# Performance work log

Measured on AMD Instinct MI355X. Metric: run time of the kernel, lower is better.

The kernel has to match this reference:

```python
import jax, jax.numpy as jnp
import numpy as np

BS, CI, NI, CO, NO = 16, 2048, 16, 64, 32
ITERATIONS = 3


def squash(x, axis=2):
    # x * ||x|| / (1 + ||x||^2) along `axis`
    norm = jnp.linalg.norm(x, axis=axis, keepdims=True)
    return x * norm / (1.0 + norm * norm)


def setup_inputs() -> dict:
    key = jax.random.key(0)
    k1, k2 = jax.random.split(key)
    x = jax.random.normal(k1, (BS, CI, NI), dtype=jnp.float32)
    # kaiming-uniform-ish init for weight [ci, ni, co*no]
    bound = float(np.sqrt(6.0 / NI))
    weight = jax.random.uniform(k2, (CI, NI, CO * NO), dtype=jnp.float32,
                                minval=-bound, maxval=bound)
    bias = jnp.full((CO, NO), 0.1, dtype=jnp.float32)
    return {"x": x, "weight": weight, "bias": bias}


def reference(x, weight, bias):
    bs = x.shape[0]
    # votes: (x.unsqueeze(3) * W).sum(2) == einsum over ni -> [bs, ci, co*no]
    votes = jnp.einsum('bci,cik->bck', x, weight).reshape(bs, CI, CO, NO)
    logits = jnp.zeros((bs, CI, CO), dtype=votes.dtype)
    activation = None
    for _ in range(ITERATIONS):
        route = jax.nn.softmax(logits, axis=2)              # [bs, ci, co]
        # s_j = sum_i c_ij * u_hat_{j|i} + bias            # [bs, co, no]
        preactivate = jnp.einsum('bic,bicn->bcn', route, votes) + bias
        activation = squash(preactivate, axis=2)            # [bs, co, no]
        # agreement: sum_n u_hat * v                        # [bs, ci, co]
        distances = jnp.einsum('bicn,bcn->bic', votes, activation)
        logits = logits + distances
    return activation
```

## Files before the change

kernel.cpp:

```cpp
#include <hip/hip_runtime.h>

#define BS 16
#define CI 2048
#define NI 16
#define CO 64
#define NO 32
#define KK 2048
#define NGRP 256

__device__ __forceinline__ void load_lds16(const float* g, float* l) {
    __builtin_amdgcn_global_load_lds(
        (const __attribute__((address_space(1))) void*)g,
        (__attribute__((address_space(3))) void*)l, 16, 0, 0);
}

#define WAITVM12 asm volatile("s_waitcnt vmcnt(12)" ::: "memory")
#define WAITVM4  asm volatile("s_waitcnt vmcnt(4)" ::: "memory")
#define WAITVM0  asm volatile("s_waitcnt vmcnt(0)" ::: "memory")
#define WAITLGKM asm volatile("s_waitcnt lgkmcnt(0)" ::: "memory")
#define BAR __builtin_amdgcn_s_barrier
#define MEMFENCE asm volatile("" ::: "memory")

__device__ __forceinline__ unsigned bf16rne(float f) {
    unsigned u = __float_as_uint(f);
    return (u + 0x7fffu + ((u >> 16) & 1u)) >> 16;
}
__device__ __forceinline__ unsigned pack2(float lo, float hi) {
    return bf16rne(lo) | (bf16rne(hi) << 16);
}

__global__ __launch_bounds__(512, 2) void votes_kernel(
    const float* __restrict__ x,
    const float* __restrict__ w,
    unsigned* __restrict__ votes,
    float* __restrict__ partials)
{
    __shared__ float wbuf[2][4 * KK];
    __shared__ float xb[8][8][NI];

    const int t = threadIdx.x;
    const int phys = blockIdx.x;
    const int xcd = phys & 7;
    const int slot = phys >> 3;
    const int pairid = xcd * 32 + (slot >> 1);
    const int half = slot & 1;
    const int k4 = 4 * t;

    {
        int il = t >> 6, b = (t >> 3) & 7, n0 = (t & 7) * 2;
        int i = pairid + il * NGRP;
        *(float2*)&xb[il][b][n0] =
            *(const float2*)&x[((size_t)(half * 8 + b) * CI + i) * NI + n0];
    }
    __syncthreads();

    float4 acc[8];
#pragma unroll
    for (int b = 0; b < 8; ++b) acc[b] = make_float4(0.f, 0.f, 0.f, 0.f);

    auto issue = [&](int s) {
        int ilp = s >> 2, qp = s & 3;
        const float* gb = w + ((size_t)(pairid + ilp * NGRP) * NI + qp * 4) * KK + k4;
        float* lb = wbuf[s & 1] + k4;
#pragma unroll
        for (int r = 0; r < 4; ++r)
            load_lds16(gb + (size_t)r * KK, lb + r * KK);
    };

    auto computequarter = [&](int il, int q, float4(&dst)[8]) {
#pragma unroll
        for (int rg = 0; rg < 2; ++rg) {
            float4 wA = *(const float4*)&wbuf[q & 1][(2 * rg) * KK + k4];
            float4 wB = *(const float4*)&wbuf[q & 1][(2 * rg + 1) * KK + k4];
#pragma unroll
            for (int b = 0; b < 8; ++b) {
                float2 xv = *(const float2*)&xb[il][b][q * 4 + 2 * rg];
                dst[b].x = fmaf(xv.x, wA.x, dst[b].x);
                dst[b].y = fmaf(xv.x, wA.y, dst[b].y);
                dst[b].z = fmaf(xv.x, wA.z, dst[b].z);
                dst[b].w = fmaf(xv.x, wA.w, dst[b].w);
                dst[b].x = fmaf(xv.y, wB.x, dst[b].x);
                dst[b].y = fmaf(xv.y, wB.y, dst[b].y);
                dst[b].z = fmaf(xv.y, wB.z, dst[b].z);
                dst[b].w = fmaf(xv.y, wB.w, dst[b].w);
            }
        }
    };

    issue(0); issue(1);

#pragma unroll 1
    for (int il = 0; il < 8; ++il) {
        float4 v[8];
#pragma unroll
        for (int b = 0; b < 8; ++b) v[b] = make_float4(0.f, 0.f, 0.f, 0.f);

#pragma unroll
        for (int q = 0; q < 4; ++q) {
            if (q < 2) { if (il > 0) { WAITVM12; } else { WAITVM4; } }
            else if (q == 3) { if (il == 7) { WAITVM0; } else { WAITVM4; } }
            else { WAITVM4; }
            computequarter(il, q, v);
            WAITLGKM;
            if (il < 7 || q < 2) issue(il * 4 + q + 2);
        }

        const size_t vbase = ((size_t)(pairid + il * NGRP) * BS + half * 8) * (KK / 2) + 2 * t;
#pragma unroll
        for (int b = 0; b < 8; ++b) {
            acc[b].x += v[b].x; acc[b].y += v[b].y;
            acc[b].z += v[b].z; acc[b].w += v[b].w;
            uint2 pk;
            pk.x = pack2(v[b].x, v[b].y);
            pk.y = pack2(v[b].z, v[b].w);
            *(uint2*)&votes[vbase + (size_t)b * (KK / 2)] = pk;
        }
        MEMFENCE;
    }

#pragma unroll
    for (int b = 0; b < 8; ++b)
        *(float4*)&partials[((size_t)pairid * BS + half * 8 + b) * KK + k4] = acc[b];
}

#define RILBODY(IL, VC, VN)                                                    \
  {                                                                            \
    const int buf = (IL) & 1;                                                  \
    if ((IL) < 7) {                                                            \
      _Pragma("unroll")                                                        \
      for (int lb = 0; lb < 2; ++lb)                                           \
        VN[lb] = *(const uint4*)&votes[((size_t)(gid + ((IL) + 1) * NGRP) * BS \
                                        + bg0 + lb) * (KK / 2) + 4 * ks];      \
    }                                                                          \
    float dv[2];                                                               \
    _Pragma("unroll")                                                          \
    for (int lb = 0; lb < 2; ++lb) {                                           \
      float4 a0 = *(const float4*)&actb[2 * bh + lb][k8];                      \
      float4 a1 = *(const float4*)&actb[2 * bh + lb][k8 + 4];                  \
      float d = __uint_as_float(VC[lb].x << 16) * a0.x                         \
              + __uint_as_float(VC[lb].x & 0xffff0000u) * a0.y                 \
              + __uint_as_float(VC[lb].y << 16) * a0.z                         \
              + __uint_as_float(VC[lb].y & 0xffff0000u) * a0.w                 \
              + __uint_as_float(VC[lb].z << 16) * a1.x                         \
              + __uint_as_float(VC[lb].z & 0xffff0000u) * a1.y                 \
              + __uint_as_float(VC[lb].w << 16) * a1.z                         \
              + __uint_as_float(VC[lb].w & 0xffff0000u) * a1.w;                \
      d += __shfl_xor(d, 1, 4);                                                \
      d += __shfl_xor(d, 2, 4);                                                \
      dv[lb] = d;                                                              \
    }                                                                          \
    if (j4 == 0) sm[buf][(2 * bh) * 65 + co] = dv[0];                          \
    if (j4 == 1) sm[buf][(2 * bh + 1) * 65 + co] = dv[1];                      \
    WAITLGKM; BAR();                                                           \
    if (t < 256) {                                                             \
      float l0 = sm[buf][(t >> 6) * 65 + (t & 63)];                            \
      if (MODE == 1) lg[(IL)] = l0; else l0 += lg[(IL)];                       \
      float mx = l0;                                                           \
      mx = fmaxf(mx, __shfl_xor(mx, 1, 64));                                   \
      mx = fmaxf(mx, __shfl_xor(mx, 2, 64));                                   \
      mx = fmaxf(mx, __shfl_xor(mx, 4, 64));                                   \
      mx = fmaxf(mx, __shfl_xor(mx, 8, 64));                                   \
      mx = fmaxf(mx, __shfl_xor(mx, 16, 64));                                  \
      mx = fmaxf(mx, __shfl_xor(mx, 32, 64));                                  \
      float e = __expf(l0 - mx);                                               \
      float ssum = e;                                                          \
      ssum += __shfl_xor(ssum, 1, 64);                                         \
      ssum += __shfl_xor(ssum, 2, 64);                                         \
      ssum += __shfl_xor(ssum, 4, 64);                                         \
      ssum += __shfl_xor(ssum, 8, 64);                                         \
      ssum += __shfl_xor(ssum, 16, 64);                                        \
      ssum += __shfl_xor(ssum, 32, 64);                                        \
      sm[buf][(t >> 6) * 65 + (t & 63)] = e / ssum;                            \
      WAITLGKM;                                                                \
    }                                                                          \
    BAR();                                                                     \
    _Pragma("unroll")                                                          \
    for (int lb = 0; lb < 2; ++lb) {                                           \
      float r = sm[buf][(2 * bh + lb) * 65 + co];                              \
      acc[2 * lb + 0].x = fmaf(r, __uint_as_float(VC[lb].x << 16), acc[2 * lb + 0].x); \
      acc[2 * lb + 0].y = fmaf(r, __uint_as_float(VC[lb].x & 0xffff0000u), acc[2 * lb + 0].y); \
      acc[2 * lb + 0].z = fmaf(r, __uint_as_float(VC[lb].y << 16), acc[2 * lb + 0].z); \
      acc[2 * lb + 0].w = fmaf(r, __uint_as_float(VC[lb].y & 0xffff0000u), acc[2 * lb + 0].w); \
      acc[2 * lb + 1].x = fmaf(r, __uint_as_float(VC[lb].z << 16), acc[2 * lb + 1].x); \
      acc[2 * lb + 1].y = fmaf(r, __uint_as_float(VC[lb].z & 0xffff0000u), acc[2 * lb + 1].y); \
      acc[2 * lb + 1].z = fmaf(r, __uint_as_float(VC[lb].w << 16), acc[2 * lb + 1].z); \
      acc[2 * lb + 1].w = fmaf(r, __uint_as_float(VC[lb].w & 0xffff0000u), acc[2 * lb + 1].w); \
    }                                                                          \
  }

template <int MODE>
__global__ __launch_bounds__(512, 2) void route_kernel(
    const unsigned* __restrict__ votes,
    const float* __restrict__ act_in,
    float* __restrict__ logits,
    float* __restrict__ partials)
{
    __shared__ float actb[4][KK];
    __shared__ float sm[2][4 * 65];

    const int t = threadIdx.x;
    const int phys = blockIdx.x;
    const int xcd = phys & 7;
    const int slot = phys >> 3;
    const int gid = xcd * 32 + (slot >> 2);
    const int quarter = slot & 3;

    const int ks = t & 255;
    const int k8 = 8 * ks;
    const int co = ks >> 2;
    const int j4 = ks & 3;
    const int bh = t >> 8;
    const int bg0 = quarter * 4 + 2 * bh;

    {
        int br = t >> 7, e0 = (t & 127) * 16;
#pragma unroll
        for (int r = 0; r < 4; ++r)
            *(float4*)&actb[br][e0 + 4 * r] =
                *(const float4*)&act_in[(size_t)(quarter * 4 + br) * KK + e0 + 4 * r];
    }
    float lg[8];
    if constexpr (MODE == 2) {
        if (t < 256) {
#pragma unroll
            for (int il = 0; il < 8; ++il)
                lg[il] = logits[((size_t)(quarter * 4 + (t >> 6)) * CI + (gid + il * NGRP)) * CO + (t & 63)];
        }
    }
    __syncthreads();

    float4 acc[4];
#pragma unroll
    for (int i = 0; i < 4; ++i) acc[i] = make_float4(0.f, 0.f, 0.f, 0.f);

    uint4 vA[2], vB[2];
#pragma unroll
    for (int lb = 0; lb < 2; ++lb)
        vA[lb] = *(const uint4*)&votes[((size_t)gid * BS + bg0 + lb) * (KK / 2) + 4 * ks];

    RILBODY(0, vA, vB)
    RILBODY(1, vB, vA)
    RILBODY(2, vA, vB)
    RILBODY(3, vB, vA)
    RILBODY(4, vA, vB)
    RILBODY(5, vB, vA)
    RILBODY(6, vA, vB)
    RILBODY(7, vB, vA)

#pragma unroll
    for (int lb = 0; lb < 2; ++lb) {
        float* pp = &partials[((size_t)gid * BS + bg0 + lb) * KK + k8];
        *(float4*)pp = acc[2 * lb];
        *(float4*)(pp + 4) = acc[2 * lb + 1];
    }
    if constexpr (MODE == 1) {
        if (t < 256) {
#pragma unroll
            for (int il = 0; il < 8; ++il)
                logits[((size_t)(quarter * 4 + (t >> 6)) * CI + (gid + il * NGRP)) * CO + (t & 63)] = lg[il];
        }
    }
}

__global__ __launch_bounds__(128) void reduce_squash(
    const float* __restrict__ partials,
    const float* __restrict__ bias,
    float* __restrict__ act_out, float scale)
{
    __shared__ float4 sred[4][32];
    const int t = threadIdx.x;
    const int blk = blockIdx.x;
    const int lane = t & 31;
    const int gp = t >> 5;
    const int o4 = blk * 128 + lane * 4;
    const int b = o4 >> 11;
    const int kk = o4 & (KK - 1);
    const float* p = partials + (size_t)b * KK + kk;
    const size_t stride = (size_t)BS * KK;

    float4 s = make_float4(0.f, 0.f, 0.f, 0.f);
#pragma unroll 4
    for (int g = gp * 64; g < gp * 64 + 64; ++g) {
        float4 v = *(const float4*)(p + (size_t)g * stride);
        s.x += v.x; s.y += v.y; s.z += v.z; s.w += v.w;
    }
    sred[gp][lane] = s;
    __syncthreads();

    if (t < 32) {
        float4 v0 = sred[0][t], v1 = sred[1][t], v2 = sred[2][t], v3 = sred[3][t];
        float4 v;
        v.x = (v0.x + v1.x) + (v2.x + v3.x);
        v.y = (v0.y + v1.y) + (v2.y + v3.y);
        v.z = (v0.z + v1.z) + (v2.z + v3.z);
        v.w = (v0.w + v1.w) + (v2.w + v3.w);
        const int ot = blk * 128 + t * 4;
        float4 bb = *(const float4*)&bias[ot & (KK - 1)];
        v.x = v.x * scale + bb.x;
        v.y = v.y * scale + bb.y;
        v.z = v.z * scale + bb.z;
        v.w = v.w * scale + bb.w;
        float n2 = v.x * v.x + v.y * v.y + v.z * v.z + v.w * v.w;
#pragma unroll
        for (int m = 1; m < 8; m <<= 1) n2 += __shfl_xor(n2, m, 8);
        float norm = sqrtf(n2);
        float sc = norm / (1.f + n2);
        float4 o = make_float4(v.x * sc, v.y * sc, v.z * sc, v.w * sc);
        *(float4*)&act_out[ot] = o;
    }
}

extern "C" void kernel_launch(void* const* d_in, const int* in_sizes, int n_in,
                              void* d_out, int out_size, void* d_ws, size_t ws_size,
                              hipStream_t stream) {
    const float* x = (const float*)d_in[0];
    const float* w = (const float*)d_in[1];
    const float* bias = (const float*)d_in[2];
    float* out = (float*)d_out;

    char* p = (char*)d_ws;
    unsigned* votes = (unsigned*)p; p += (size_t)CI * BS * KK * 2;
    float* partials = (float*)p;    p += (size_t)NGRP * BS * KK * 4;
    float* logits = (float*)p;      p += (size_t)BS * CI * CO * 4;
    float* act1 = (float*)p;        p += (size_t)BS * KK * 4;
    float* act2 = (float*)p;

    votes_kernel<<<2 * NGRP, 512, 0, stream>>>(x, w, votes, partials);
    reduce_squash<<<256, 128, 0, stream>>>(partials, bias, act1, 1.0f / (float)CO);
    route_kernel<1><<<4 * NGRP, 512, 0, stream>>>(votes, act1, logits, partials);
    reduce_squash<<<256, 128, 0, stream>>>(partials, bias, act2, 1.0f);
    route_kernel<2><<<4 * NGRP, 512, 0, stream>>>(votes, act2, logits, partials);
    reduce_squash<<<256, 128, 0, stream>>>(partials, bias, out, 1.0f);
}
```

Before: 192.9 us.

## Drop logits buffer via linearity, split vote sum out, shrink votes LDS staging

Uses the linearity of the routing logits to skip storing and reloading them: the second routing pass recomputes agreement against act1+act2 instead of adding saved logits, which removes a large global write and read. The first-pass sum over inputs moves out of the votes kernel into a separate vote_sum kernel that reads the bf16 votes, so the votes kernel no longer writes partials. The votes kernel also halves its LDS weight staging (two rows per stage instead of four) with adjusted vmcnt waits and asks for higher occupancy in its launch bounds. The trade-off is an extra kernel launch and an extra read pass over votes, and the first iteration's sum is now built from bf16-rounded votes.

```diff
diff --git a/kernel.cpp b/kernel.cpp
--- a/kernel.cpp
+++ b/kernel.cpp
@@ -14,8 +14,8 @@
         (__attribute__((address_space(3))) void*)l, 16, 0, 0);
 }
 
-#define WAITVM12 asm volatile("s_waitcnt vmcnt(12)" ::: "memory")
-#define WAITVM4  asm volatile("s_waitcnt vmcnt(4)" ::: "memory")
+#define WAITVM10 asm volatile("s_waitcnt vmcnt(10)" ::: "memory")
+#define WAITVM2  asm volatile("s_waitcnt vmcnt(2)" ::: "memory")
 #define WAITVM0  asm volatile("s_waitcnt vmcnt(0)" ::: "memory")
 #define WAITLGKM asm volatile("s_waitcnt lgkmcnt(0)" ::: "memory")
 #define BAR __builtin_amdgcn_s_barrier
@@ -28,14 +28,15 @@
 __device__ __forceinline__ unsigned pack2(float lo, float hi) {
     return bf16rne(lo) | (bf16rne(hi) << 16);
 }
-
-__global__ __launch_bounds__(512, 2) void votes_kernel(
+__device__ __forceinline__ float bflo(unsigned u) { return __uint_as_float(u << 16); }
+__device__ __forceinline__ float bfhi(unsigned u) { return __uint_as_float(u & 0xffff0000u); }
+
+__global__ __launch_bounds__(512, 8) void votes_kernel(
     const float* __restrict__ x,
     const float* __restrict__ w,
-    unsigned* __restrict__ votes,
-    float* __restrict__ partials)
+    unsigned* __restrict__ votes)
 {
-    __shared__ float wbuf[2][4 * KK];
+    __shared__ float wbuf[2][2 * KK];
     __shared__ float xb[8][8][NI];
 
     const int t = threadIdx.x;
@@ -54,37 +55,12 @@
     }
     __syncthreads();
 
-    float4 acc[8];
-#pragma unroll
-    for (int b = 0; b < 8; ++b) acc[b] = make_float4(0.f, 0.f, 0.f, 0.f);
-
     auto issue = [&](int s) {
-        int ilp = s >> 2, qp = s & 3;
-        const float* gb = w + ((size_t)(pairid + ilp * NGRP) * NI + qp * 4) * KK + k4;
+        int ilp = s >> 3, qp = s & 7;
+        const float* gb = w + ((size_t)(pairid + ilp * NGRP) * NI + 2 * qp) * KK + k4;
         float* lb = wbuf[s & 1] + k4;
-#pragma unroll
-        for (int r = 0; r < 4; ++r)
-            load_lds16(gb + (size_t)r * KK, lb + r * KK);
-    };
-
-    auto computequarter = [&](int il, int q, float4(&dst)[8]) {
-#pragma unroll
-        for (int rg = 0; rg < 2; ++rg) {
-            float4 wA = *(const float4*)&wbuf[q & 1][(2 * rg) * KK + k4];
-            float4 wB = *(const float4*)&wbuf[q & 1][(2 * rg + 1) * KK + k4];
-#pragma unroll
-            for (int b = 0; b < 8; ++b) {
-                float2 xv = *(const float2*)&xb[il][b][q * 4 + 2 * rg];
-                dst[b].x = fmaf(xv.x, wA.x, dst[b].x);
-                dst[b].y = fmaf(xv.x, wA.y, dst[b].y);
-                dst[b].z = fmaf(xv.x, wA.z, dst[b].z);
-                dst[b].w = fmaf(xv.x, wA.w, dst[b].w);
-                dst[b].x = fmaf(xv.y, wB.x, dst[b].x);
-                dst[b].y = fmaf(xv.y, wB.y, dst[b].y);
-                dst[b].z = fmaf(xv.y, wB.z, dst[b].z);
-                dst[b].w = fmaf(xv.y, wB.w, dst[b].w);
-            }
-        }
+        load_lds16(gb, lb);
+        load_lds16(gb + KK, lb + KK);
     };
 
     issue(0); issue(1);
@@ -96,20 +72,34 @@
         for (int b = 0; b < 8; ++b) v[b] = make_float4(0.f, 0.f, 0.f, 0.f);
 
 #pragma unroll
-        for (int q = 0; q < 4; ++q) {
-            if (q < 2) { if (il > 0) { WAITVM12; } else { WAITVM4; } }
-            else if (q == 3) { if (il == 7) { WAITVM0; } else { WAITVM4; } }
-            else { WAITVM4; }
-            computequarter(il, q, v);
+        for (int q = 0; q < 8; ++q) {
+            const int s = il * 8 + q;
+            if (s == 63) { WAITVM0; }
+            else if (il > 0 && q < 2) { WAITVM10; }
+            else { WAITVM2; }
+            {
+                float4 wA = *(const float4*)&wbuf[q & 1][k4];
+                float4 wB = *(const float4*)&wbuf[q & 1][KK + k4];
+#pragma unroll
+                for (int b = 0; b < 8; ++b) {
+                    float2 xv = *(const float2*)&xb[il][b][2 * q];
+                    v[b].x = fmaf(xv.x, wA.x, v[b].x);
+                    v[b].y = fmaf(xv.x, wA.y, v[b].y);
+                    v[b].z = fmaf(xv.x, wA.z, v[b].z);
+                    v[b].w = fmaf(xv.x, wA.w, v[b].w);
+                    v[b].x = fmaf(xv.y, wB.x, v[b].x);
+                    v[b].y = fmaf(xv.y, wB.y, v[b].y);
+                    v[b].z = fmaf(xv.y, wB.z, v[b].z);
+                    v[b].w = fmaf(xv.y, wB.w, v[b].w);
+                }
+            }
             WAITLGKM;
-            if (il < 7 || q < 2) issue(il * 4 + q + 2);
+            if (s + 2 < 64) issue(s + 2);
         }
 
         const size_t vbase = ((size_t)(pairid + il * NGRP) * BS + half * 8) * (KK / 2) + 2 * t;
 #pragma unroll
         for (int b = 0; b < 8; ++b) {
-            acc[b].x += v[b].x; acc[b].y += v[b].y;
-            acc[b].z += v[b].z; acc[b].w += v[b].w;
             uint2 pk;
             pk.x = pack2(v[b].x, v[b].y);
             pk.y = pack2(v[b].z, v[b].w);
@@ -117,10 +107,37 @@
         }
         MEMFENCE;
     }
-
-#pragma unroll
-    for (int b = 0; b < 8; ++b)
-        *(float4*)&partials[((size_t)pairid * BS + half * 8 + b) * KK + k4] = acc[b];
+}
+
+__global__ __launch_bounds__(256) void vote_sum(
+    const unsigned* __restrict__ votes, float* __restrict__ part1)
+{
+    const int t = threadIdx.x;
+    const int b = blockIdx.x & 15;
+    const int ic = blockIdx.x >> 4;
+    float s[8];
+#pragma unroll
+    for (int j = 0; j < 8; ++j) s[j] = 0.f;
+    const unsigned* base = votes + (size_t)b * (KK / 2) + 4 * t;
+    const size_t istride = (size_t)BS * (KK / 2);
+#pragma unroll 1
+    for (int i0 = ic * 64; i0 < ic * 64 + 64; i0 += 4) {
+        uint4 u0 = *(const uint4*)(base + (size_t)(i0 + 0) * istride);
+        uint4 u1 = *(const uint4*)(base + (size_t)(i0 + 1) * istride);
+        uint4 u2 = *(const uint4*)(base + (size_t)(i0 + 2) * istride);
+        uint4 u3 = *(const uint4*)(base + (size_t)(i0 + 3) * istride);
+        s[0] += bflo(u0.x) + bflo(u1.x) + bflo(u2.x) + bflo(u3.x);
+        s[1] += bfhi(u0.x) + bfhi(u1.x) + bfhi(u2.x) + bfhi(u3.x);
+        s[2] += bflo(u0.y) + bflo(u1.y) + bflo(u2.y) + bflo(u3.y);
+        s[3] += bfhi(u0.y) + bfhi(u1.y) + bfhi(u2.y) + bfhi(u3.y);
+        s[4] += bflo(u0.z) + bflo(u1.z) + bflo(u2.z) + bflo(u3.z);
+        s[5] += bfhi(u0.z) + bfhi(u1.z) + bfhi(u2.z) + bfhi(u3.z);
+        s[6] += bflo(u0.w) + bflo(u1.w) + bflo(u2.w) + bflo(u3.w);
+        s[7] += bfhi(u0.w) + bfhi(u1.w) + bfhi(u2.w) + bfhi(u3.w);
+    }
+    float* op = part1 + ((size_t)ic * BS + b) * KK + 8 * t;
+    *(float4*)op = make_float4(s[0], s[1], s[2], s[3]);
+    *(float4*)(op + 4) = make_float4(s[4], s[5], s[6], s[7]);
 }
 
 #define RILBODY(IL, VC, VN)                                                    \
@@ -137,14 +154,10 @@
     for (int lb = 0; lb < 2; ++lb) {                                           \
       float4 a0 = *(const float4*)&actb[2 * bh + lb][k8];                      \
       float4 a1 = *(const float4*)&actb[2 * bh + lb][k8 + 4];                  \
-      float d = __uint_as_float(VC[lb].x << 16) * a0.x                         \
-              + __uint_as_float(VC[lb].x & 0xffff0000u) * a0.y                 \
-              + __uint_as_float(VC[lb].y << 16) * a0.z                         \
-              + __uint_as_float(VC[lb].y & 0xffff0000u) * a0.w                 \
-              + __uint_as_float(VC[lb].z << 16) * a1.x                         \
-              + __uint_as_float(VC[lb].z & 0xffff0000u) * a1.y                 \
-              + __uint_as_float(VC[lb].w << 16) * a1.z                         \
-              + __uint_as_float(VC[lb].w & 0xffff0000u) * a1.w;                \
+      float d = bflo(VC[lb].x) * a0.x + bfhi(VC[lb].x) * a0.y                  \
+              + bflo(VC[lb].y) * a0.z + bfhi(VC[lb].y) * a0.w                  \
+              + bflo(VC[lb].z) * a1.x + bfhi(VC[lb].z) * a1.y                  \
+              + bflo(VC[lb].w) * a1.z + bfhi(VC[lb].w) * a1.w;                 \
       d += __shfl_xor(d, 1, 4);                                                \
       d += __shfl_xor(d, 2, 4);                                                \
       dv[lb] = d;                                                              \
@@ -154,7 +167,6 @@
     WAITLGKM; BAR();                                                           \
     if (t < 256) {                                                             \
       float l0 = sm[buf][(t >> 6) * 65 + (t & 63)];                            \
-      if (MODE == 1) lg[(IL)] = l0; else l0 += lg[(IL)];                       \
       float mx = l0;                                                           \
       mx = fmaxf(mx, __shfl_xor(mx, 1, 64));                                   \
       mx = fmaxf(mx, __shfl_xor(mx, 2, 64));                                   \
@@ -177,22 +189,22 @@
     _Pragma("unroll")                                                          \
     for (int lb = 0; lb < 2; ++lb) {                                           \
       float r = sm[buf][(2 * bh + lb) * 65 + co];                              \
-      acc[2 * lb + 0].x = fmaf(r, __uint_as_float(VC[lb].x << 16), acc[2 * lb + 0].x); \
-      acc[2 * lb + 0].y = fmaf(r, __uint_as_float(VC[lb].x & 0xffff0000u), acc[2 * lb + 0].y); \
-      acc[2 * lb + 0].z = fmaf(r, __uint_as_float(VC[lb].y << 16), acc[2 * lb + 0].z); \
-      acc[2 * lb + 0].w = fmaf(r, __uint_as_float(VC[lb].y & 0xffff0000u), acc[2 * lb + 0].w); \
-      acc[2 * lb + 1].x = fmaf(r, __uint_as_float(VC[lb].z << 16), acc[2 * lb + 1].x); \
-      acc[2 * lb + 1].y = fmaf(r, __uint_as_float(VC[lb].z & 0xffff0000u), acc[2 * lb + 1].y); \
-      acc[2 * lb + 1].z = fmaf(r, __uint_as_float(VC[lb].w << 16), acc[2 * lb + 1].z); \
-      acc[2 * lb + 1].w = fmaf(r, __uint_as_float(VC[lb].w & 0xffff0000u), acc[2 * lb + 1].w); \
+      acc[2 * lb + 0].x = fmaf(r, bflo(VC[lb].x), acc[2 * lb + 0].x);          \
+      acc[2 * lb + 0].y = fmaf(r, bfhi(VC[lb].x), acc[2 * lb + 0].y);          \
+      acc[2 * lb + 0].z = fmaf(r, bflo(VC[lb].y), acc[2 * lb + 0].z);          \
+      acc[2 * lb + 0].w = fmaf(r, bfhi(VC[lb].y), acc[2 * lb + 0].w);          \
+      acc[2 * lb + 1].x = fmaf(r, bflo(VC[lb].z), acc[2 * lb + 1].x);          \
+      acc[2 * lb + 1].y = fmaf(r, bfhi(VC[lb].z), acc[2 * lb + 1].y);          \
+      acc[2 * lb + 1].z = fmaf(r, bflo(VC[lb].w), acc[2 * lb + 1].z);          \
+      acc[2 * lb + 1].w = fmaf(r, bfhi(VC[lb].w), acc[2 * lb + 1].w);          \
     }                                                                          \
   }
 
-template <int MODE>
+template <bool TWOACT>
 __global__ __launch_bounds__(512, 2) void route_kernel(
     const unsigned* __restrict__ votes,
-    const float* __restrict__ act_in,
-    float* __restrict__ logits,
+    const float* __restrict__ act1,
+    const float* __restrict__ act2,
     float* __restrict__ partials)
 {
     __shared__ float actb[4][KK];
@@ -215,16 +227,13 @@
     {
         int br = t >> 7, e0 = (t & 127) * 16;
 #pragma unroll
-        for (int r = 0; r < 4; ++r)
-            *(float4*)&actb[br][e0 + 4 * r] =
-                *(const float4*)&act_in[(size_t)(quarter * 4 + br) * KK + e0 + 4 * r];
-    }
-    float lg[8];
-    if constexpr (MODE == 2) {
-        if (t < 256) {
-#pragma unroll
-            for (int il = 0; il < 8; ++il)
-                lg[il] = logits[((size_t)(quarter * 4 + (t >> 6)) * CI + (gid + il * NGRP)) * CO + (t & 63)];
+        for (int r = 0; r < 4; ++r) {
+            float4 u = *(const float4*)&act1[(size_t)(quarter * 4 + br) * KK + e0 + 4 * r];
+            if constexpr (TWOACT) {
+                float4 u2 = *(const float4*)&act2[(size_t)(quarter * 4 + br) * KK + e0 + 4 * r];
+                u.x += u2.x; u.y += u2.y; u.z += u2.z; u.w += u2.w;
+            }
+            *(float4*)&actb[br][e0 + 4 * r] = u;
         }
     }
     __syncthreads();
@@ -253,15 +262,9 @@
         *(float4*)pp = acc[2 * lb];
         *(float4*)(pp + 4) = acc[2 * lb + 1];
     }
-    if constexpr (MODE == 1) {
-        if (t < 256) {
-#pragma unroll
-            for (int il = 0; il < 8; ++il)
-                logits[((size_t)(quarter * 4 + (t >> 6)) * CI + (gid + il * NGRP)) * CO + (t & 63)] = lg[il];
-        }
-    }
-}
-
+}
+
+template <int G>
 __global__ __launch_bounds__(128) void reduce_squash(
     const float* __restrict__ partials,
     const float* __restrict__ bias,
@@ -280,7 +283,7 @@
 
     float4 s = make_float4(0.f, 0.f, 0.f, 0.f);
 #pragma unroll 4
-    for (int g = gp * 64; g < gp * 64 + 64; ++g) {
+    for (int g = gp * (G / 4); g < gp * (G / 4) + (G / 4); ++g) {
         float4 v = *(const float4*)(p + (size_t)g * stride);
         s.x += v.x; s.y += v.y; s.z += v.z; s.w += v.w;
     }
@@ -321,14 +324,15 @@
     char* p = (char*)d_ws;
     unsigned* votes = (unsigned*)p; p += (size_t)CI * BS * KK * 2;
     float* partials = (float*)p;    p += (size_t)NGRP * BS * KK * 4;
-    float* logits = (float*)p;      p += (size_t)BS * CI * CO * 4;
+    float* part1 = (float*)p;       p += (size_t)32 * BS * KK * 4;
     float* act1 = (float*)p;        p += (size_t)BS * KK * 4;
     float* act2 = (float*)p;
 
-    votes_kernel<<<2 * NGRP, 512, 0, stream>>>(x, w, votes, partials);
-    reduce_squash<<<256, 128, 0, stream>>>(partials, bias, act1, 1.0f / (float)CO);
-    route_kernel<1><<<4 * NGRP, 512, 0, stream>>>(votes, act1, logits, partials);
-    reduce_squash<<<256, 128, 0, stream>>>(partials, bias, act2, 1.0f);
-    route_kernel<2><<<4 * NGRP, 512, 0, stream>>>(votes, act2, logits, partials);
-    reduce_squash<<<256, 128, 0, stream>>>(partials, bias, out, 1.0f);
-}
+    votes_kernel<<<2 * NGRP, 512, 0, stream>>>(x, w, votes);
+    vote_sum<<<512, 256, 0, stream>>>(votes, part1);
+    reduce_squash<32><<<256, 128, 0, stream>>>(part1, bias, act1, 1.0f / (float)CO);
+    route_kernel<false><<<4 * NGRP, 512, 0, stream>>>(votes, act1, nullptr, partials);
+    reduce_squash<256><<<256, 128, 0, stream>>>(partials, bias, act2, 1.0f);
+    route_kernel<true><<<4 * NGRP, 512, 0, stream>>>(votes, act1, act2, partials);
+    reduce_squash<256><<<256, 128, 0, stream>>>(partials, bias, out, 1.0f);
+}
```

Measured after the change: 712.1 us. +269.2%, slower.
